# Kernel tuning notes

Measured on AMD Instinct MI355X. Metric: run time of the kernel, lower is better.

Reference implementation:

```python
import jax, jax.numpy as jnp
import numpy as np
import math

E_IN, E_OUT = 512, 96
B, QL, PL = 64, 128, 196

def _lin(k, shape):
    fan_in = shape[1]
    bound = 1.0 / math.sqrt(fan_in)
    k1, k2 = jax.random.split(k)
    W = jax.random.uniform(k1, shape, jnp.float32, -bound, bound)
    b = jax.random.uniform(k2, (shape[0],), jnp.float32, -bound, bound)
    return W, b

def setup_inputs() -> dict:
    key = jax.random.key(0)
    ks = jax.random.split(key, 16)
    inp = {
        'z_d_cls': jax.random.normal(ks[0], (B, E_IN), jnp.float32),
        'Z_d_tok': jax.random.normal(ks[1], (B, QL, E_IN), jnp.float32),
        'z_t_cls': jax.random.normal(ks[2], (B, E_IN), jnp.float32),
        'Z_t_tok': jax.random.normal(ks[3], (B, QL, E_IN), jnp.float32),
        'z_v_cls': jax.random.normal(ks[4], (B, E_IN), jnp.float32),
        'Z_v_patch': jax.random.normal(ks[5], (B, PL, E_IN), jnp.float32),
    }
    names = ['t_cls', 'd_cls', 'v_cls', 't_tok', 'v_patch', 'tgl_q', 'tgl_k', 'tgl_v']
    for i, n in enumerate(names):
        W, b = _lin(ks[6 + i], (E_OUT, E_IN))
        inp[f'W_{n}'] = W
        inp[f'b_{n}'] = b
    inp['ln_g'] = jnp.ones((E_OUT,), jnp.float32)
    inp['ln_b'] = jnp.zeros((E_OUT,), jnp.float32)
    return inp

def _l2n(x, eps=1e-6):
    return x / jnp.maximum(jnp.linalg.norm(x, axis=-1, keepdims=True), eps)

def _proj(x, W, b):
    return x @ W.T + b

def _layer_norm(x, g, b, eps=1e-5):
    mu = jnp.mean(x, axis=-1, keepdims=True)
    var = jnp.mean((x - mu) ** 2, axis=-1, keepdims=True)
    return (x - mu) / jnp.sqrt(var + eps) * g + b

def reference(z_d_cls, Z_d_tok, z_t_cls, Z_t_tok, z_v_cls, Z_v_patch,
              W_t_cls, b_t_cls, W_d_cls, b_d_cls, W_v_cls, b_v_cls,
              W_t_tok, b_t_tok, W_v_patch, b_v_patch,
              W_tgl_q, b_tgl_q, W_tgl_k, b_tgl_k, W_tgl_v, b_tgl_v,
              ln_g, ln_b):
    # --- TGG: global-global text/doc cosine sim [B, B]
    t = _l2n(_proj(z_t_cls, W_t_cls, b_t_cls))
    d = _l2n(_proj(z_d_cls, W_d_cls, b_d_cls))
    S_TGG = t @ d.T
    # --- TGL: cross-attention over all batch pairs
    Q = _proj(Z_d_tok, W_tgl_q, b_tgl_q)   # [b, q, h]
    K = _proj(Z_t_tok, W_tgl_k, b_tgl_k)   # [c, k, h]
    V = _proj(Z_t_tok, W_tgl_v, b_tgl_v)   # [c, k, h]
    scores = jnp.einsum('bqh,ckh->bcqk', Q, K) / math.sqrt(E_OUT)
    attn = jax.nn.softmax(scores, axis=-1)
    context = jnp.einsum('bcqk,ckh->bcqh', attn, V).mean(axis=2)  # [b, c, h]
    context = _layer_norm(context, ln_g, ln_b)
    S_TGL = jnp.einsum('ih,ijh->ij', d, _l2n(context))
    S_TIB = 0.5 * (S_TGG + S_TGL)
    # --- CGG: global-global text/vision cosine sim
    v = _l2n(_proj(z_v_cls, W_v_cls, b_v_cls))
    S_CGG = t @ v.T
    # --- CLL: token-patch max similarity
    t_tok = _l2n(_proj(Z_t_tok, W_t_tok, b_t_tok))        # [b, t, h]
    v_pat = _l2n(_proj(Z_v_patch, W_v_patch, b_v_patch))  # [c, p, h]
    sim = jnp.einsum('bth,cph->bctp', t_tok, v_pat)
    S_CLL = sim.max(axis=(-1, -2))
    S_CAB = 0.5 * (S_CGG + S_CLL)
    return S_TIB + S_CAB
```

## Files before the change

kernel.cpp:

```cpp
#include <hip/hip_runtime.h>
#include <hip/hip_bf16.h>
#include <math.h>

typedef __bf16 bf16;
typedef __attribute__((ext_vector_type(8))) __bf16 bf16x8;
typedef __attribute__((ext_vector_type(2))) float f32x2;
typedef __attribute__((ext_vector_type(4))) float f32x4;
typedef __attribute__((ext_vector_type(4))) unsigned int uint4v;

#define MFMA16(a, b, c) __builtin_amdgcn_mfma_f32_16x16x32_bf16(a, b, c, 0, 0, 0)

#define QSCALE 0.14724450f

__device__ inline bf16x8 cvt8(const float* p) {
    f32x4 lo = *(const f32x4*)p;
    f32x4 hi = *(const f32x4*)(p + 4);
    bf16x8 r;
    r[0] = (bf16)lo[0]; r[1] = (bf16)lo[1]; r[2] = (bf16)lo[2]; r[3] = (bf16)lo[3];
    r[4] = (bf16)hi[0]; r[5] = (bf16)hi[1]; r[6] = (bf16)hi[2]; r[7] = (bf16)hi[3];
    return r;
}


struct WPtrs { const float* W[8]; };

__global__ __launch_bounds__(256) void cvtw_kernel(WPtrs wp, bf16* __restrict__ Wb) {
    int j   = blockIdx.x / 48;
    int blk = blockIdx.x - j * 48;
    int idx = (blk * 256 + threadIdx.x) * 4;
    f32x4 v = *(const f32x4*)(wp.W[j] + idx);
    bf16* dst = Wb + j * 49152 + idx;
    dst[0] = (bf16)v[0]; dst[1] = (bf16)v[1]; dst[2] = (bf16)v[2]; dst[3] = (bf16)v[3];
}


struct ProjParams {
    const float* src[8];
    const float* B[8];
    void* dst[8];
    const bf16* Wb;
};

__global__ __launch_bounds__(128, 4) void proj_kernel(ProjParams p) {
    int g   = blockIdx.x;
    int tid = threadIdx.x;
    int nh = tid >> 6, lane = tid & 63;
    int m = lane & 15, quad = lane >> 4;

    int job = 0, base = 0;
    if (g >= 2)    { job = 1; base = 2; }
    if (g >= 4)    { job = 2; base = 4; }
    if (g >= 6)    { job = 3; base = 6; }
    if (g >= 262)  { job = 4; base = 262; }
    if (g >= 518)  { job = 5; base = 518; }
    if (g >= 774)  { job = 6; base = 774; }
    if (g >= 1030) { job = 7; base = 1030; }
    int r0 = (g - base) << 5;

    const float* X  = p.src[job];
    const bf16*  wb = p.Wb + job * 49152 + (size_t)(nh * 48 + m) * 512 + quad * 8;
    const float* x0 = X + (size_t)(r0 + m) * 512 + quad * 8;
    const float* x1 = x0 + 16 * 512;

    f32x4 acc[2][3] = {};
    #pragma unroll 4
    for (int kk = 0; kk < 512; kk += 32) {
        bf16x8 a0 = cvt8(x0 + kk);
        bf16x8 a1 = cvt8(x1 + kk);
        #pragma unroll
        for (int nt = 0; nt < 3; nt++) {
            bf16x8 b = *(const bf16x8*)(wb + nt * 8192 + kk);
            acc[0][nt] = MFMA16(a0, b, acc[0][nt]);
            acc[1][nt] = MFMA16(a1, b, acc[1][nt]);
        }
    }
    const float* Bv = p.B[job];
    #pragma unroll
    for (int t2 = 0; t2 < 2; t2++)
        #pragma unroll
        for (int nt = 0; nt < 3; nt++) {
            float bb = Bv[nh * 48 + nt * 16 + m];
            acc[t2][nt][0] += bb; acc[t2][nt][1] += bb;
            acc[t2][nt][2] += bb; acc[t2][nt][3] += bb;
        }

    bool norm = (job < 3) || (job >= 6);
    __shared__ float sx[2][2][16];
    if (norm) {
        float ss[2][4];
        #pragma unroll
        for (int t2 = 0; t2 < 2; t2++)
            #pragma unroll
            for (int r = 0; r < 4; r++) {
                float s = 0.0f;
                #pragma unroll
                for (int nt = 0; nt < 3; nt++) s += acc[t2][nt][r] * acc[t2][nt][r];
                s += __shfl_xor(s, 1); s += __shfl_xor(s, 2);
                s += __shfl_xor(s, 4); s += __shfl_xor(s, 8);
                ss[t2][r] = s;
            }
        if (m == 0) {
            #pragma unroll
            for (int t2 = 0; t2 < 2; t2++)
                #pragma unroll
                for (int r = 0; r < 4; r++)
                    sx[nh][t2][quad * 4 + r] = ss[t2][r];
        }
        __syncthreads();
        #pragma unroll
        for (int t2 = 0; t2 < 2; t2++)
            #pragma unroll
            for (int r = 0; r < 4; r++) {
                float tot = ss[t2][r] + sx[1 - nh][t2][quad * 4 + r];
                float inv = 1.0f / fmaxf(sqrtf(tot), 1e-6f);
                #pragma unroll
                for (int nt = 0; nt < 3; nt++) acc[t2][nt][r] *= inv;
            }
    } else if (job == 3) {
        #pragma unroll
        for (int t2 = 0; t2 < 2; t2++)
            #pragma unroll
            for (int nt = 0; nt < 3; nt++) {
                acc[t2][nt][0] *= QSCALE; acc[t2][nt][1] *= QSCALE;
                acc[t2][nt][2] *= QSCALE; acc[t2][nt][3] *= QSCALE;
            }
    }
    if (job < 3) {
        float* dst = (float*)p.dst[job];
        #pragma unroll
        for (int t2 = 0; t2 < 2; t2++)
            #pragma unroll
            for (int r = 0; r < 4; r++)
                #pragma unroll
                for (int nt = 0; nt < 3; nt++)
                    dst[(size_t)(r0 + t2 * 16 + quad * 4 + r) * 96 + nh * 48 + nt * 16 + m] = acc[t2][nt][r];
    } else {
        bf16* dst = (bf16*)p.dst[job];
        #pragma unroll
        for (int t2 = 0; t2 < 2; t2++)
            #pragma unroll
            for (int r = 0; r < 4; r++)
                #pragma unroll
                for (int nt = 0; nt < 3; nt++)
                    dst[(size_t)(r0 + t2 * 16 + quad * 4 + r) * 96 + nh * 48 + nt * 16 + m] = (bf16)acc[t2][nt][r];
    }
}


__global__ __launch_bounds__(256) void attn_kernel(
    const bf16* __restrict__ Qg, const bf16* __restrict__ Kg, const bf16* __restrict__ Vg,
    float* __restrict__ Ctx)
{
    int pr = blockIdx.x;
    int b = pr >> 6, c = pr & 63;
    int tid = threadIdx.x, lane = tid & 63, w = tid >> 6;
    int m = lane & 15, quad = lane >> 4;
    const bf16* Q = Qg + (size_t)b * (128 * 96);
    const bf16* K = Kg + (size_t)c * (128 * 96);
    const bf16* V = Vg + (size_t)c * (128 * 96);

    __shared__ __align__(16) bf16 Klds[128 * 104];
    #pragma unroll
    for (int it = 0; it < 6; it++) {
        int ch = it * 256 + tid;
        int row = ch / 12, seg = ch - row * 12;
        *(uint4v*)(Klds + row * 104 + seg * 8) = *(const uint4v*)(K + ch * 8);
    }
    __syncthreads();

    f32x4 acc[2][8] = {};
    #pragma unroll
    for (int kk = 0; kk < 96; kk += 32) {
        bf16x8 a0 = *(const bf16x8*)(Q + (size_t)(w * 32 + m) * 96 + kk + quad * 8);
        bf16x8 a1 = *(const bf16x8*)(Q + (size_t)(w * 32 + 16 + m) * 96 + kk + quad * 8);
        #pragma unroll
        for (int nt = 0; nt < 8; nt++) {
            bf16x8 bb = *(const bf16x8*)(Klds + (nt * 16 + m) * 104 + kk + quad * 8);
            acc[0][nt] = MFMA16(a0, bb, acc[0][nt]);
            acc[1][nt] = MFMA16(a1, bb, acc[1][nt]);
        }
    }
    float wpart[8];
    #pragma unroll
    for (int nt = 0; nt < 8; nt++) wpart[nt] = 0.0f;
    #pragma unroll
    for (int mt = 0; mt < 2; mt++) {
        #pragma unroll
        for (int r = 0; r < 4; r++) {
            float tv[8]; float s = 0.0f;
            #pragma unroll
            for (int nt = 0; nt < 8; nt++) { tv[nt] = exp2f(acc[mt][nt][r]); s += tv[nt]; }
            s += __shfl_xor(s, 1); s += __shfl_xor(s, 2);
            s += __shfl_xor(s, 4); s += __shfl_xor(s, 8);
            float inv = 1.0f / s;
            #pragma unroll
            for (int nt = 0; nt < 8; nt++) wpart[nt] += tv[nt] * inv;
        }
    }
    #pragma unroll
    for (int nt = 0; nt < 8; nt++) {
        wpart[nt] += __shfl_xor(wpart[nt], 16);
        wpart[nt] += __shfl_xor(wpart[nt], 32);
    }
    __shared__ float wsum4[4][128];
    __shared__ float wk[128];
    __shared__ float ctxp[4][96];
    if (lane < 16) {
        #pragma unroll
        for (int nt = 0; nt < 8; nt++) wsum4[w][nt * 16 + lane] = wpart[nt];
    }
    __syncthreads();
    if (tid < 128) wk[tid] = wsum4[0][tid] + wsum4[1][tid] + wsum4[2][tid] + wsum4[3][tid];
    __syncthreads();
    {
        float c0 = 0.0f, c1 = 0.0f;
        if (lane < 48) {
            #pragma unroll 4
            for (int r = 0; r < 32; r++) {
                int k = w * 32 + r;
                unsigned u = *(const unsigned*)(V + (size_t)k * 96 + lane * 2);
                float lo = __uint_as_float(u << 16);
                float hi = __uint_as_float(u & 0xffff0000u);
                float wkk = wk[k];
                c0 += wkk * lo; c1 += wkk * hi;
            }
            ctxp[w][lane * 2]     = c0;
            ctxp[w][lane * 2 + 1] = c1;
        }
    }
    __syncthreads();
    if (tid < 96)
        Ctx[(size_t)pr * 96 + tid] =
            (ctxp[0][tid] + ctxp[1][tid] + ctxp[2][tid] + ctxp[3][tid]) * (1.0f / 128.0f);
}


__global__ __launch_bounds__(256) void cll_kernel(
    const bf16* __restrict__ Tt, const bf16* __restrict__ Vp, float* __restrict__ S_CLL)
{
    int c = blockIdx.x >> 3, bg = blockIdx.x & 7;
    int tid = threadIdx.x, lane = tid & 63, w = tid >> 6;
    int m = lane & 15, quad = lane >> 4;
    const bf16* P = Vp + (size_t)c * (196 * 96);

    __shared__ __align__(16) bf16 Plds[196 * 104];
    __shared__ float red[8][4];
    for (int ch = tid; ch < 2352; ch += 256) {
        int row = ch / 12, seg = ch - row * 12;
        *(uint4v*)(Plds + row * 104 + seg * 8) = *(const uint4v*)(P + ch * 8);
    }
    int rofs[13];
    #pragma unroll
    for (int nt = 0; nt < 13; nt++) {
        int r = nt * 16 + m; if (r > 195) r = 195;
        rofs[nt] = r * 104;
    }
    __syncthreads();

    for (int bi = 0; bi < 8; bi++) {
        const bf16* T = Tt + (size_t)(bg * 8 + bi) * (128 * 96);
        f32x4 acc[2][13] = {};
        #pragma unroll
        for (int kk = 0; kk < 96; kk += 32) {
            bf16x8 a0 = *(const bf16x8*)(T + (size_t)(w * 32 + m) * 96 + kk + quad * 8);
            bf16x8 a1 = *(const bf16x8*)(T + (size_t)(w * 32 + 16 + m) * 96 + kk + quad * 8);
            #pragma unroll
            for (int nt = 0; nt < 13; nt++) {
                bf16x8 bb = *(const bf16x8*)(Plds + rofs[nt] + kk + quad * 8);
                acc[0][nt] = MFMA16(a0, bb, acc[0][nt]);
                acc[1][nt] = MFMA16(a1, bb, acc[1][nt]);
            }
        }
        float mx = -3.4e38f;
        #pragma unroll
        for (int mt = 0; mt < 2; mt++)
            #pragma unroll
            for (int nt = 0; nt < 13; nt++)
                #pragma unroll
                for (int r = 0; r < 4; r++) mx = fmaxf(mx, acc[mt][nt][r]);
        #pragma unroll
        for (int d = 1; d < 64; d <<= 1) mx = fmaxf(mx, __shfl_xor(mx, d));
        if (lane == 0) red[bi][w] = mx;
    }
    __syncthreads();
    if (tid < 8)
        S_CLL[(size_t)(bg * 8 + tid) * 64 + c] =
            fmaxf(fmaxf(red[tid][0], red[tid][1]), fmaxf(red[tid][2], red[tid][3]));
}


__global__ __launch_bounds__(256) void epi_kernel(
    const float* __restrict__ Ctx, const float* __restrict__ t, const float* __restrict__ d,
    const float* __restrict__ v, const float* __restrict__ S_CLL,
    const float* __restrict__ ln_g, const float* __restrict__ ln_b,
    float* __restrict__ out)
{
    int pr = blockIdx.x * 4 + (threadIdx.x >> 6);
    int lane = threadIdx.x & 63;
    int i = pr >> 6, j = pr & 63;
    bool act = lane < 48;

    float c0 = 0, c1 = 0, t0 = 0, t1 = 0;
    float dj0 = 0, dj1 = 0, di0 = 0, di1 = 0, v0 = 0, v1 = 0, g0 = 0, g1 = 0, bb0 = 0, bb1 = 0;
    if (act) {
        f32x2 cc  = *(const f32x2*)(Ctx + (size_t)pr * 96 + lane * 2);
        f32x2 tt  = *(const f32x2*)(t + i * 96 + lane * 2);
        f32x2 ddj = *(const f32x2*)(d + j * 96 + lane * 2);
        f32x2 ddi = *(const f32x2*)(d + i * 96 + lane * 2);
        f32x2 vv  = *(const f32x2*)(v + j * 96 + lane * 2);
        f32x2 gg  = *(const f32x2*)(ln_g + lane * 2);
        f32x2 bbv = *(const f32x2*)(ln_b + lane * 2);
        c0 = cc[0]; c1 = cc[1]; t0 = tt[0]; t1 = tt[1];
        dj0 = ddj[0]; dj1 = ddj[1]; di0 = ddi[0]; di1 = ddi[1];
        v0 = vv[0]; v1 = vv[1];
        g0 = gg[0]; g1 = gg[1]; bb0 = bbv[0]; bb1 = bbv[1];
    }
    float s = c0 + c1;
    #pragma unroll
    for (int k = 1; k < 64; k <<= 1) s += __shfl_xor(s, k);
    float mean = s * (1.0f / 96.0f);
    float e0 = act ? (c0 - mean) : 0.0f;
    float e1 = act ? (c1 - mean) : 0.0f;
    float q = e0 * e0 + e1 * e1;
    #pragma unroll
    for (int k = 1; k < 64; k <<= 1) q += __shfl_xor(q, k);
    float rstd = rsqrtf(q * (1.0f / 96.0f) + 1e-5f);
    float y0 = act ? (e0 * rstd * g0 + bb0) : 0.0f;
    float y1 = act ? (e1 * rstd * g1 + bb1) : 0.0f;
    float dot = y0 * di0 + y1 * di1;
    float ssq = y0 * y0 + y1 * y1;
    float tg  = t0 * dj0 + t1 * dj1;
    float cg  = t0 * v0 + t1 * v1;
    #pragma unroll
    for (int k = 1; k < 64; k <<= 1) {
        dot += __shfl_xor(dot, k); ssq += __shfl_xor(ssq, k);
        tg  += __shfl_xor(tg, k);  cg  += __shfl_xor(cg, k);
    }
    if (lane == 0) {
        float stgl = dot / fmaxf(sqrtf(ssq), 1e-6f);
        out[pr] = 0.5f * (tg + stgl) + 0.5f * (cg + S_CLL[pr]);
    }
}


extern "C" void kernel_launch(void* const* d_in, const int* in_sizes, int n_in,
                              void* d_out, int out_size, void* d_ws, size_t ws_size,
                              hipStream_t stream)
{
    (void)in_sizes; (void)n_in; (void)out_size; (void)ws_size;
    char* ws = (char*)d_ws;
    float* t     = (float*)(ws + 0);
    float* d     = (float*)(ws + 24576);
    float* v     = (float*)(ws + 49152);
    float* S_CLL = (float*)(ws + 90112);
    bf16* Wb = (bf16*)(ws + 106496);
    bf16* Qb = (bf16*)(ws + 892928);
    bf16* Kb = (bf16*)(ws + 892928 + 1572864);
    bf16* Vb = (bf16*)(ws + 892928 + 2 * 1572864);
    bf16* Tt = (bf16*)(ws + 892928 + 3 * 1572864);
    bf16* Vp = (bf16*)(ws + 892928 + 4 * 1572864);
    float* Ctx = (float*)(ws + 892928 + 4 * 1572864 + 2408448);

    WPtrs wp;
    wp.W[0] = (const float*)d_in[6];
    wp.W[1] = (const float*)d_in[8];
    wp.W[2] = (const float*)d_in[10];
    wp.W[3] = (const float*)d_in[16];
    wp.W[4] = (const float*)d_in[18];
    wp.W[5] = (const float*)d_in[20];
    wp.W[6] = (const float*)d_in[12];
    wp.W[7] = (const float*)d_in[14];
    hipLaunchKernelGGL(cvtw_kernel, dim3(384), dim3(256), 0, stream, wp, Wb);

    ProjParams pp;
    pp.Wb = Wb;
    pp.src[0] = (const float*)d_in[2];  pp.B[0] = (const float*)d_in[7];  pp.dst[0] = t;
    pp.src[1] = (const float*)d_in[0];  pp.B[1] = (const float*)d_in[9];  pp.dst[1] = d;
    pp.src[2] = (const float*)d_in[4];  pp.B[2] = (const float*)d_in[11]; pp.dst[2] = v;
    pp.src[3] = (const float*)d_in[1];  pp.B[3] = (const float*)d_in[17]; pp.dst[3] = Qb;
    pp.src[4] = (const float*)d_in[3];  pp.B[4] = (const float*)d_in[19]; pp.dst[4] = Kb;
    pp.src[5] = (const float*)d_in[3];  pp.B[5] = (const float*)d_in[21]; pp.dst[5] = Vb;
    pp.src[6] = (const float*)d_in[3];  pp.B[6] = (const float*)d_in[13]; pp.dst[6] = Tt;
    pp.src[7] = (const float*)d_in[5];  pp.B[7] = (const float*)d_in[15]; pp.dst[7] = Vp;
    hipLaunchKernelGGL(proj_kernel, dim3(1422), dim3(128), 0, stream, pp);

    hipLaunchKernelGGL(attn_kernel, dim3(4096), dim3(256), 0, stream,
                       (const bf16*)Qb, (const bf16*)Kb, (const bf16*)Vb, Ctx);
    hipLaunchKernelGGL(cll_kernel, dim3(512), dim3(256), 0, stream,
                       (const bf16*)Tt, (const bf16*)Vp, S_CLL);
    hipLaunchKernelGGL(epi_kernel, dim3(1024), dim3(256), 0, stream,
                       (const float*)Ctx, (const float*)t, (const float*)d, (const float*)v,
                       (const float*)S_CLL, (const float*)d_in[22], (const float*)d_in[23],
                       (float*)d_out);
}
```

Measured before the change: 240.7 us.

## Split-K projection across four waves and reuse Q fragments across four c's in attention

The projection kernel now uses 256 threads, with two waves per N half each covering half of K. Partial accumulators are combined through shared memory before the bias, normalisation and store steps, which adds memory-level parallelism but also an extra barrier and LDS round trip. The attention kernel now handles four c indices per block, loading the Q fragments into registers once and looping over K/V tiles. This cuts redundant Q loads and block count, at the cost of serialising four tiles inside each block and lowering parallelism to 1024 blocks.

```diff
diff --git a/kernel.cpp b/kernel.cpp
--- a/kernel.cpp
+++ b/kernel.cpp
@@ -41,10 +41,12 @@
     const bf16* Wb;
 };
 
-__global__ __launch_bounds__(128, 4) void proj_kernel(ProjParams p) {
+__global__ __launch_bounds__(256) void proj_kernel(ProjParams p) {
     int g   = blockIdx.x;
     int tid = threadIdx.x;
-    int nh = tid >> 6, lane = tid & 63;
+    int w2 = tid >> 6;
+    int nh = w2 & 1, kh = w2 >> 1;
+    int lane = tid & 63;
     int m = lane & 15, quad = lane >> 4;
 
     int job = 0, base = 0;
@@ -58,13 +60,13 @@
     int r0 = (g - base) << 5;
 
     const float* X  = p.src[job];
-    const bf16*  wb = p.Wb + job * 49152 + (size_t)(nh * 48 + m) * 512 + quad * 8;
-    const float* x0 = X + (size_t)(r0 + m) * 512 + quad * 8;
+    const bf16*  wb = p.Wb + job * 49152 + (size_t)(nh * 48 + m) * 512 + kh * 256 + quad * 8;
+    const float* x0 = X + (size_t)(r0 + m) * 512 + kh * 256 + quad * 8;
     const float* x1 = x0 + 16 * 512;
 
     f32x4 acc[2][3] = {};
-    #pragma unroll 4
-    for (int kk = 0; kk < 512; kk += 32) {
+    #pragma unroll
+    for (int kk = 0; kk < 256; kk += 32) {
         bf16x8 a0 = cvt8(x0 + kk);
         bf16x8 a1 = cvt8(x1 + kk);
         #pragma unroll
@@ -74,75 +76,98 @@
             acc[1][nt] = MFMA16(a1, b, acc[1][nt]);
         }
     }
+
+    __shared__ float red[2 * 64 * 24];
+    __shared__ float sx[2][2][16];
+    float* myred = red + (nh * 64 + lane) * 24;
+    if (kh) {
+        #pragma unroll
+        for (int t2 = 0; t2 < 2; t2++)
+            #pragma unroll
+            for (int nt = 0; nt < 3; nt++)
+                *(f32x4*)(myred + (t2 * 3 + nt) * 4) = acc[t2][nt];
+    }
+    __syncthreads();
+
+    bool norm = (job < 3) || (job >= 6);
     const float* Bv = p.B[job];
-    #pragma unroll
-    for (int t2 = 0; t2 < 2; t2++)
-        #pragma unroll
-        for (int nt = 0; nt < 3; nt++) {
-            float bb = Bv[nh * 48 + nt * 16 + m];
-            acc[t2][nt][0] += bb; acc[t2][nt][1] += bb;
-            acc[t2][nt][2] += bb; acc[t2][nt][3] += bb;
-        }
-
-    bool norm = (job < 3) || (job >= 6);
-    __shared__ float sx[2][2][16];
-    if (norm) {
-        float ss[2][4];
+    if (!kh) {
         #pragma unroll
         for (int t2 = 0; t2 < 2; t2++)
             #pragma unroll
-            for (int r = 0; r < 4; r++) {
-                float s = 0.0f;
-                #pragma unroll
-                for (int nt = 0; nt < 3; nt++) s += acc[t2][nt][r] * acc[t2][nt][r];
-                s += __shfl_xor(s, 1); s += __shfl_xor(s, 2);
-                s += __shfl_xor(s, 4); s += __shfl_xor(s, 8);
-                ss[t2][r] = s;
-            }
-        if (m == 0) {
+            for (int nt = 0; nt < 3; nt++) {
+                f32x4 o = *(const f32x4*)(myred + (t2 * 3 + nt) * 4);
+                float bb = Bv[nh * 48 + nt * 16 + m];
+                acc[t2][nt][0] += o[0] + bb; acc[t2][nt][1] += o[1] + bb;
+                acc[t2][nt][2] += o[2] + bb; acc[t2][nt][3] += o[3] + bb;
+            }
+        if (norm) {
+            float ss[2][4];
             #pragma unroll
             for (int t2 = 0; t2 < 2; t2++)
                 #pragma unroll
+                for (int r = 0; r < 4; r++) {
+                    float s = 0.0f;
+                    #pragma unroll
+                    for (int nt = 0; nt < 3; nt++) s += acc[t2][nt][r] * acc[t2][nt][r];
+                    s += __shfl_xor(s, 1); s += __shfl_xor(s, 2);
+                    s += __shfl_xor(s, 4); s += __shfl_xor(s, 8);
+                    ss[t2][r] = s;
+                }
+            if (m == 0) {
+                #pragma unroll
+                for (int t2 = 0; t2 < 2; t2++)
+                    #pragma unroll
+                    for (int r = 0; r < 4; r++)
+                        sx[nh][t2][quad * 4 + r] = ss[t2][r];
+            }
+        }
+    }
+    __syncthreads();
+    if (!kh) {
+        if (norm) {
+            #pragma unroll
+            for (int t2 = 0; t2 < 2; t2++)
+                #pragma unroll
+                for (int r = 0; r < 4; r++) {
+                    float s = 0.0f;
+                    #pragma unroll
+                    for (int nt = 0; nt < 3; nt++) s += acc[t2][nt][r] * acc[t2][nt][r];
+                    s += __shfl_xor(s, 1); s += __shfl_xor(s, 2);
+                    s += __shfl_xor(s, 4); s += __shfl_xor(s, 8);
+                    float tot = s + sx[1 - nh][t2][quad * 4 + r];
+                    float inv = 1.0f / fmaxf(sqrtf(tot), 1e-6f);
+                    #pragma unroll
+                    for (int nt = 0; nt < 3; nt++) acc[t2][nt][r] *= inv;
+                }
+        } else if (job == 3) {
+            #pragma unroll
+            for (int t2 = 0; t2 < 2; t2++)
+                #pragma unroll
+                for (int nt = 0; nt < 3; nt++) {
+                    acc[t2][nt][0] *= QSCALE; acc[t2][nt][1] *= QSCALE;
+                    acc[t2][nt][2] *= QSCALE; acc[t2][nt][3] *= QSCALE;
+                }
+        }
+        if (job < 3) {
+            float* dst = (float*)p.dst[job];
+            #pragma unroll
+            for (int t2 = 0; t2 < 2; t2++)
+                #pragma unroll
                 for (int r = 0; r < 4; r++)
-                    sx[nh][t2][quad * 4 + r] = ss[t2][r];
-        }
-        __syncthreads();
-        #pragma unroll
-        for (int t2 = 0; t2 < 2; t2++)
-            #pragma unroll
-            for (int r = 0; r < 4; r++) {
-                float tot = ss[t2][r] + sx[1 - nh][t2][quad * 4 + r];
-                float inv = 1.0f / fmaxf(sqrtf(tot), 1e-6f);
-                #pragma unroll
-                for (int nt = 0; nt < 3; nt++) acc[t2][nt][r] *= inv;
-            }
-    } else if (job == 3) {
-        #pragma unroll
-        for (int t2 = 0; t2 < 2; t2++)
-            #pragma unroll
-            for (int nt = 0; nt < 3; nt++) {
-                acc[t2][nt][0] *= QSCALE; acc[t2][nt][1] *= QSCALE;
-                acc[t2][nt][2] *= QSCALE; acc[t2][nt][3] *= QSCALE;
-            }
-    }
-    if (job < 3) {
-        float* dst = (float*)p.dst[job];
-        #pragma unroll
-        for (int t2 = 0; t2 < 2; t2++)
-            #pragma unroll
-            for (int r = 0; r < 4; r++)
-                #pragma unroll
-                for (int nt = 0; nt < 3; nt++)
-                    dst[(size_t)(r0 + t2 * 16 + quad * 4 + r) * 96 + nh * 48 + nt * 16 + m] = acc[t2][nt][r];
-    } else {
-        bf16* dst = (bf16*)p.dst[job];
-        #pragma unroll
-        for (int t2 = 0; t2 < 2; t2++)
-            #pragma unroll
-            for (int r = 0; r < 4; r++)
-                #pragma unroll
-                for (int nt = 0; nt < 3; nt++)
-                    dst[(size_t)(r0 + t2 * 16 + quad * 4 + r) * 96 + nh * 48 + nt * 16 + m] = (bf16)acc[t2][nt][r];
+                    #pragma unroll
+                    for (int nt = 0; nt < 3; nt++)
+                        dst[(size_t)(r0 + t2 * 16 + quad * 4 + r) * 96 + nh * 48 + nt * 16 + m] = acc[t2][nt][r];
+        } else {
+            bf16* dst = (bf16*)p.dst[job];
+            #pragma unroll
+            for (int t2 = 0; t2 < 2; t2++)
+                #pragma unroll
+                for (int r = 0; r < 4; r++)
+                    #pragma unroll
+                    for (int nt = 0; nt < 3; nt++)
+                        dst[(size_t)(r0 + t2 * 16 + quad * 4 + r) * 96 + nh * 48 + nt * 16 + m] = (bf16)acc[t2][nt][r];
+        }
     }
 }
 
@@ -151,87 +176,96 @@
     const bf16* __restrict__ Qg, const bf16* __restrict__ Kg, const bf16* __restrict__ Vg,
     float* __restrict__ Ctx)
 {
-    int pr = blockIdx.x;
-    int b = pr >> 6, c = pr & 63;
+    int b  = blockIdx.x >> 4;
+    int cg = blockIdx.x & 15;
     int tid = threadIdx.x, lane = tid & 63, w = tid >> 6;
     int m = lane & 15, quad = lane >> 4;
     const bf16* Q = Qg + (size_t)b * (128 * 96);
-    const bf16* K = Kg + (size_t)c * (128 * 96);
-    const bf16* V = Vg + (size_t)c * (128 * 96);
+
+    bf16x8 qa0[3], qa1[3];
+    #pragma unroll
+    for (int i = 0; i < 3; i++) {
+        qa0[i] = *(const bf16x8*)(Q + (size_t)(w * 32 + m) * 96 + i * 32 + quad * 8);
+        qa1[i] = *(const bf16x8*)(Q + (size_t)(w * 32 + 16 + m) * 96 + i * 32 + quad * 8);
+    }
 
     __shared__ __align__(16) bf16 Klds[128 * 104];
-    #pragma unroll
-    for (int it = 0; it < 6; it++) {
-        int ch = it * 256 + tid;
-        int row = ch / 12, seg = ch - row * 12;
-        *(uint4v*)(Klds + row * 104 + seg * 8) = *(const uint4v*)(K + ch * 8);
-    }
-    __syncthreads();
-
-    f32x4 acc[2][8] = {};
-    #pragma unroll
-    for (int kk = 0; kk < 96; kk += 32) {
-        bf16x8 a0 = *(const bf16x8*)(Q + (size_t)(w * 32 + m) * 96 + kk + quad * 8);
-        bf16x8 a1 = *(const bf16x8*)(Q + (size_t)(w * 32 + 16 + m) * 96 + kk + quad * 8);
-        #pragma unroll
-        for (int nt = 0; nt < 8; nt++) {
-            bf16x8 bb = *(const bf16x8*)(Klds + (nt * 16 + m) * 104 + kk + quad * 8);
-            acc[0][nt] = MFMA16(a0, bb, acc[0][nt]);
-            acc[1][nt] = MFMA16(a1, bb, acc[1][nt]);
-        }
-    }
-    float wpart[8];
-    #pragma unroll
-    for (int nt = 0; nt < 8; nt++) wpart[nt] = 0.0f;
-    #pragma unroll
-    for (int mt = 0; mt < 2; mt++) {
-        #pragma unroll
-        for (int r = 0; r < 4; r++) {
-            float tv[8]; float s = 0.0f;
-            #pragma unroll
-            for (int nt = 0; nt < 8; nt++) { tv[nt] = exp2f(acc[mt][nt][r]); s += tv[nt]; }
-            s += __shfl_xor(s, 1); s += __shfl_xor(s, 2);
-            s += __shfl_xor(s, 4); s += __shfl_xor(s, 8);
-            float inv = 1.0f / s;
-            #pragma unroll
-            for (int nt = 0; nt < 8; nt++) wpart[nt] += tv[nt] * inv;
-        }
-    }
-    #pragma unroll
-    for (int nt = 0; nt < 8; nt++) {
-        wpart[nt] += __shfl_xor(wpart[nt], 16);
-        wpart[nt] += __shfl_xor(wpart[nt], 32);
-    }
     __shared__ float wsum4[4][128];
     __shared__ float wk[128];
     __shared__ float ctxp[4][96];
-    if (lane < 16) {
-        #pragma unroll
-        for (int nt = 0; nt < 8; nt++) wsum4[w][nt * 16 + lane] = wpart[nt];
-    }
-    __syncthreads();
-    if (tid < 128) wk[tid] = wsum4[0][tid] + wsum4[1][tid] + wsum4[2][tid] + wsum4[3][tid];
-    __syncthreads();
-    {
-        float c0 = 0.0f, c1 = 0.0f;
-        if (lane < 48) {
-            #pragma unroll 4
-            for (int r = 0; r < 32; r++) {
-                int k = w * 32 + r;
-                unsigned u = *(const unsigned*)(V + (size_t)k * 96 + lane * 2);
-                float lo = __uint_as_float(u << 16);
-                float hi = __uint_as_float(u & 0xffff0000u);
-                float wkk = wk[k];
-                c0 += wkk * lo; c1 += wkk * hi;
-            }
-            ctxp[w][lane * 2]     = c0;
-            ctxp[w][lane * 2 + 1] = c1;
-        }
-    }
-    __syncthreads();
-    if (tid < 96)
-        Ctx[(size_t)pr * 96 + tid] =
-            (ctxp[0][tid] + ctxp[1][tid] + ctxp[2][tid] + ctxp[3][tid]) * (1.0f / 128.0f);
+
+    for (int ci = 0; ci < 4; ci++) {
+        int c = cg * 4 + ci;
+        const bf16* K = Kg + (size_t)c * (128 * 96);
+        const bf16* V = Vg + (size_t)c * (128 * 96);
+        #pragma unroll
+        for (int it = 0; it < 6; it++) {
+            int ch = it * 256 + tid;
+            int row = ch / 12, seg = ch - row * 12;
+            *(uint4v*)(Klds + row * 104 + seg * 8) = *(const uint4v*)(K + ch * 8);
+        }
+        __syncthreads();
+
+        f32x4 acc[2][8] = {};
+        #pragma unroll
+        for (int kki = 0; kki < 3; kki++) {
+            #pragma unroll
+            for (int nt = 0; nt < 8; nt++) {
+                bf16x8 bb = *(const bf16x8*)(Klds + (nt * 16 + m) * 104 + kki * 32 + quad * 8);
+                acc[0][nt] = MFMA16(qa0[kki], bb, acc[0][nt]);
+                acc[1][nt] = MFMA16(qa1[kki], bb, acc[1][nt]);
+            }
+        }
+        float wpart[8];
+        #pragma unroll
+        for (int nt = 0; nt < 8; nt++) wpart[nt] = 0.0f;
+        #pragma unroll
+        for (int mt = 0; mt < 2; mt++) {
+            #pragma unroll
+            for (int r = 0; r < 4; r++) {
+                float tv[8]; float s = 0.0f;
+                #pragma unroll
+                for (int nt = 0; nt < 8; nt++) { tv[nt] = exp2f(acc[mt][nt][r]); s += tv[nt]; }
+                s += __shfl_xor(s, 1); s += __shfl_xor(s, 2);
+                s += __shfl_xor(s, 4); s += __shfl_xor(s, 8);
+                float inv = 1.0f / s;
+                #pragma unroll
+                for (int nt = 0; nt < 8; nt++) wpart[nt] += tv[nt] * inv;
+            }
+        }
+        #pragma unroll
+        for (int nt = 0; nt < 8; nt++) {
+            wpart[nt] += __shfl_xor(wpart[nt], 16);
+            wpart[nt] += __shfl_xor(wpart[nt], 32);
+        }
+        if (lane < 16) {
+            #pragma unroll
+            for (int nt = 0; nt < 8; nt++) wsum4[w][nt * 16 + lane] = wpart[nt];
+        }
+        __syncthreads();
+        if (tid < 128) wk[tid] = wsum4[0][tid] + wsum4[1][tid] + wsum4[2][tid] + wsum4[3][tid];
+        __syncthreads();
+        {
+            float c0 = 0.0f, c1 = 0.0f;
+            if (lane < 48) {
+                #pragma unroll 4
+                for (int r = 0; r < 32; r++) {
+                    int k = w * 32 + r;
+                    unsigned u = *(const unsigned*)(V + (size_t)k * 96 + lane * 2);
+                    float lo = __uint_as_float(u << 16);
+                    float hi = __uint_as_float(u & 0xffff0000u);
+                    float wkk = wk[k];
+                    c0 += wkk * lo; c1 += wkk * hi;
+                }
+                ctxp[w][lane * 2]     = c0;
+                ctxp[w][lane * 2 + 1] = c1;
+            }
+        }
+        __syncthreads();
+        if (tid < 96)
+            Ctx[(size_t)(b * 64 + c) * 96 + tid] =
+                (ctxp[0][tid] + ctxp[1][tid] + ctxp[2][tid] + ctxp[3][tid]) * (1.0f / 128.0f);
+    }
 }
 
 
@@ -382,9 +416,9 @@
     pp.src[5] = (const float*)d_in[3];  pp.B[5] = (const float*)d_in[21]; pp.dst[5] = Vb;
     pp.src[6] = (const float*)d_in[3];  pp.B[6] = (const float*)d_in[13]; pp.dst[6] = Tt;
     pp.src[7] = (const float*)d_in[5];  pp.B[7] = (const float*)d_in[15]; pp.dst[7] = Vp;
-    hipLaunchKernelGGL(proj_kernel, dim3(1422), dim3(128), 0, stream, pp);
-
-    hipLaunchKernelGGL(attn_kernel, dim3(4096), dim3(256), 0, stream,
+    hipLaunchKernelGGL(proj_kernel, dim3(1422), dim3(256), 0, stream, pp);
+
+    hipLaunchKernelGGL(attn_kernel, dim3(1024), dim3(256), 0, stream,
                        (const bf16*)Qb, (const bf16*)Kb, (const bf16*)Vb, Ctx);
     hipLaunchKernelGGL(cll_kernel, dim3(512), dim3(256), 0, stream,
                        (const bf16*)Tt, (const bf16*)Vp, S_CLL);
```

New measurement: 260.2 us. 1.08x slower.
